# Kernel tuning notes

Measured on AMD Instinct MI355X. Metric: run time of the kernel, lower is better.

Reference implementation:

```python
import jax, jax.numpy as jnp
import numpy as np
import itertools
from jax import lax

B, DIM, RES = 32, 256, 8
KEY_DIM, NUM_HEADS, ATTN_RATIO = 16, 8, 4
NH_KD = KEY_DIM * NUM_HEADS          # 128
DH = ATTN_RATIO * KEY_DIM * NUM_HEADS  # 512
HQKV = DH + 2 * NH_KD                # 768
N = RES ** 3                         # 512


def _bias_idxs():
    pts = np.array(list(itertools.product(range(RES), repeat=3)))  # [N,3]
    off = np.abs(pts[:, None, :] - pts[None, :, :])                # [N,N,3]
    return jnp.asarray(off[..., 0] * RES * RES + off[..., 1] * RES + off[..., 2], dtype=jnp.int32)


def setup_inputs() -> dict:
    key = jax.random.key(0)
    ks = jax.random.split(key, 12)
    s = 0.05
    return {
        "x": jax.random.normal(ks[0], (B, DIM, RES, RES, RES), jnp.float32),
        "qkv_w": jax.random.normal(ks[1], (HQKV, DIM), jnp.float32) * s,
        "qkv_scale": jax.random.uniform(ks[2], (HQKV,), jnp.float32, 0.5, 1.5),
        "qkv_bias": jax.random.normal(ks[3], (HQKV,), jnp.float32) * s,
        "dw_w": jax.random.normal(ks[4], (NH_KD, 1, 3, 3, 3), jnp.float32) * s,
        "dw_scale": jax.random.uniform(ks[5], (NH_KD,), jnp.float32, 0.5, 1.5),
        "dw_bias": jax.random.normal(ks[6], (NH_KD,), jnp.float32) * s,
        "attn_biases": jax.random.normal(ks[7], (NUM_HEADS, N), jnp.float32) * s,
        "proj_w": jax.random.normal(ks[8], (DIM, DH), jnp.float32) * s,
        "proj_scale": jax.random.uniform(ks[9], (DIM,), jnp.float32, 0.5, 1.5),
        "proj_bias": jax.random.normal(ks[10], (DIM,), jnp.float32) * s,
        "bias_idxs": _bias_idxs(),
    }


def _cbn(x, w, scale, bias):
    # 1x1x1 Conv3d (pointwise, no bias) + folded BatchNorm (per-channel affine)
    y = jnp.einsum('bcdhw,oc->bodhw', x, w)
    return y * scale[None, :, None, None, None] + bias[None, :, None, None, None]


def reference(x, qkv_w, qkv_scale, qkv_bias, dw_w, dw_scale, dw_bias,
              attn_biases, proj_w, proj_scale, proj_bias, bias_idxs):
    Bx, _, D, H, W = x.shape
    n = D * H * W
    scale = KEY_DIM ** -0.5

    qkv = _cbn(x, qkv_w, qkv_scale, qkv_bias)  # [B, 768, D,H,W]
    q = qkv[:, :NH_KD]
    k = qkv[:, NH_KD:2 * NH_KD]
    v = qkv[:, 2 * NH_KD:]

    # depthwise 3x3x3 conv on q + folded BN
    q = lax.conv_general_dilated(q, dw_w, (1, 1, 1), [(1, 1)] * 3,
                                 dimension_numbers=('NCDHW', 'OIDHW', 'NCDHW'),
                                 feature_group_count=NH_KD)
    q = q * dw_scale[None, :, None, None, None] + dw_bias[None, :, None, None, None]

    q = q.reshape(Bx, NUM_HEADS, KEY_DIM, n)
    k = k.reshape(Bx, NUM_HEADS, KEY_DIM, n)
    v = v.reshape(Bx, NUM_HEADS, DH // NUM_HEADS, n)

    attn = jnp.einsum('bhcn,bhcm->bhnm', q, k) * scale
    attn = attn + attn_biases[:, bias_idxs]          # gathered rel-pos bias [h,N,N]
    attn = jax.nn.softmax(attn, axis=-1)

    out = jnp.einsum('bhdm,bhnm->bhdn', v, attn)     # v @ attn^T
    out = out.reshape(Bx, DH, D, H, W)
    out = jax.nn.relu(out)
    return _cbn(out, proj_w, proj_scale, proj_bias)
```

## Files before the change

kernel.cpp:

```cpp
#include <hip/hip_runtime.h>

typedef unsigned int u32;
typedef unsigned short u16;
typedef __attribute__((ext_vector_type(8))) short bf16x8;
typedef __attribute__((ext_vector_type(4))) float f32x4;

constexpr int BATCH = 32;
constexpr int DIM   = 256;
constexpr int NPTS  = 512;
constexpr int NH    = 8;
constexpr int KD    = 16;
constexpr int DHEAD = 64;
constexpr int NH_KD = 128;
constexpr int DH    = 512;

__device__ __forceinline__ float bflo(u32 u){ return __uint_as_float(u << 16); }
__device__ __forceinline__ float bfhi(u32 u){ return __uint_as_float(u & 0xffff0000u); }
__device__ __forceinline__ float bf2f(u16 u){ return __uint_as_float(((u32)u) << 16); }

__device__ __forceinline__ u32 pack2bf(float a, float b){
  u32 r;
  asm("v_cvt_pk_bf16_f32 %0, %1, %2" : "=v"(r) : "v"(a), "v"(b));
  return r;
}
__device__ __forceinline__ u16 f2bf(float f){ return (u16)pack2bf(f, f); }

union B8 { bf16x8 v; uint2 u2[2]; uint4 u4; };

typedef const __attribute__((address_space(1))) unsigned int gu32_t;
typedef __attribute__((address_space(3))) unsigned int su32_t;
__device__ __forceinline__ void gld16(const u16* src, u16* ldsDst){
  __builtin_amdgcn_global_load_lds((gu32_t*)src, (su32_t*)ldsDst, 16, 0, 0);
}

__global__ __launch_bounds__(256) void k_pre(
    const float* __restrict__ wq, const float* __restrict__ sq,
    const float* __restrict__ wp, const float* __restrict__ sp,
    u32* __restrict__ wqb, u32* __restrict__ pwb,
    const float* __restrict__ x, u16* __restrict__ xbt,
    const float* __restrict__ ab, const int* __restrict__ bidx,
    u32* __restrict__ biasb)
{
  __shared__ u16 T[64*68];
  const int blk = blockIdx.x;
  const int tid = threadIdx.x;

  if (blk < 640){
    int t = blk * 256 + tid;
    if (t < 98304){
      int i = 2*t;
      float s = sq[i >> 8];
      wqb[t] = pack2bf(wq[i]*s, wq[i+1]*s);
    } else {
      int j = t - 98304;
      int i = 2*j;
      float s = sp[i >> 9];
      pwb[j] = pack2bf(wp[i]*s, wp[i+1]*s);
    }
  } else if (blk < 1664){
    const int bk = blk - 640;
    const int b = bk >> 5, ct = (bk >> 3) & 3, nt = bk & 7;
    const int c0 = ct*64, n0 = nt*64;

    const float* xb = x + ((size_t)b*DIM + c0)*NPTS + n0;
    #pragma unroll
    for (int it = 0; it < 4; it++){
      int cc = (tid >> 4) + it*16;
      int nn = (tid & 15) * 4;
      float4 v = *(const float4*)(xb + (size_t)cc*NPTS + nn);
      u32* dst = (u32*)&T[cc*68 + nn];
      dst[0] = pack2bf(v.x, v.y);
      dst[1] = pack2bf(v.z, v.w);
    }
    __syncthreads();
    u16* ob = xbt + ((size_t)b*NPTS + n0)*DIM + c0;
    #pragma unroll
    for (int it = 0; it < 4; it++){
      int nn = (tid >> 4) + it*16;
      int cc = (tid & 15) * 4;
      uint2 w;
      w.x = (u32)T[(cc+0)*68 + nn] | ((u32)T[(cc+1)*68 + nn] << 16);
      w.y = (u32)T[(cc+2)*68 + nn] | ((u32)T[(cc+3)*68 + nn] << 16);
      *(uint2*)(ob + (size_t)nn*DIM + cc) = w;
    }
  } else {
    const float L2E = 1.4426950408889634f;
    const int bk = blk - 1664;
    const int mtg = bk >> 5, ntile = bk & 31;
    const int lane = tid & 63;
    const int h0 = tid >> 6;
    const int qq = lane >> 4;
    const int n = ntile*16 + (lane & 15);
    int idx[4];
    #pragma unroll
    for (int r = 0; r < 4; r++)
      idx[r] = bidx[(size_t)n*NPTS + mtg*16 + qq*4 + r];
    for (int h = h0; h < NH; h += 4){
      float v0 = ab[h*NPTS + idx[0]] * L2E, v1 = ab[h*NPTS + idx[1]] * L2E;
      float v2 = ab[h*NPTS + idx[2]] * L2E, v3 = ab[h*NPTS + idx[3]] * L2E;
      u32* dst = biasb + (((size_t)(h*32 + mtg)*32 + ntile)*64 + lane)*2;
      dst[0] = pack2bf(v0, v1);
      dst[1] = pack2bf(v2, v3);
    }
  }
}

__global__ __launch_bounds__(256) void k_qkv(
    const u16* __restrict__ xbt, const u16* __restrict__ wqb,
    const float* __restrict__ bias,
    u16* __restrict__ qfb, u16* __restrict__ kb, u16* __restrict__ vb)
{
  __shared__ u16 As[2][4096];
  __shared__ u16 Bs[2][4096];

  const int Mblk = blockIdx.x, Nblk = blockIdx.y, b = blockIdx.z;
  const int tid = threadIdx.x, wave = tid >> 6, lane = tid & 63;
  const int wm = wave >> 1, wn = wave & 1;
  const int c = lane & 15, q = lane >> 4;
  const int Mbase = Mblk*128 + wm*64;

  f32x4 acc[4][4];
  #pragma unroll
  for (int mt = 0; mt < 4; mt++){
    f32x4 bi;
    #pragma unroll
    for (int r = 0; r < 4; r++) bi[r] = bias[Mbase + mt*16 + q*4 + r];
    #pragma unroll
    for (int nt = 0; nt < 4; nt++) acc[mt][nt] = bi;
  }

  const u16* aT = wqb + (size_t)(Mblk*128)*DIM;
  const u16* bT = xbt + ((size_t)b*NPTS + Nblk*128)*DIM;

  const int srow = lane >> 2, scol = (lane & 3)*8;
  const int ch0 = wave*2;

  auto STAGE = [&](int buf, int kc){
    #pragma unroll
    for (int i = 0; i < 2; i++){
      const int ch = ch0 + i;
      gld16(aT + (size_t)(ch*16 + srow)*DIM + kc + scol, &As[buf][ch*512]);
      gld16(bT + (size_t)(ch*16 + srow)*DIM + kc + scol, &Bs[buf][ch*512]);
    }
  };

  STAGE(0, 0);
  __syncthreads();

  int cur = 0;
  #pragma unroll 2
  for (int ks = 0; ks < 8; ks++){
    if (ks < 7) STAGE(cur^1, (ks+1)*32);
    bf16x8 aW[4], bX[4];
    #pragma unroll
    for (int mt = 0; mt < 4; mt++)
      aW[mt] = *(const bf16x8*)&As[cur][(wm*64 + mt*16 + c)*32 + q*8];
    #pragma unroll
    for (int nt = 0; nt < 4; nt++)
      bX[nt] = *(const bf16x8*)&Bs[cur][(wn*64 + nt*16 + c)*32 + q*8];
    #pragma unroll
    for (int mt = 0; mt < 4; mt++)
      #pragma unroll
      for (int nt = 0; nt < 4; nt++)
        acc[mt][nt] = __builtin_amdgcn_mfma_f32_16x16x32_bf16(
            aW[mt], bX[nt], acc[mt][nt], 0, 0, 0);
    __syncthreads();
    cur ^= 1;
  }

  #pragma unroll
  for (int mt = 0; mt < 4; mt++){
    const int ob = wm*64 + mt*16 + q*4;
    #pragma unroll
    for (int nt = 0; nt < 4; nt++){
      const int n = Nblk*128 + wn*64 + nt*16 + c;
      #pragma unroll
      for (int r = 0; r < 4; r++){
        u16 bv = f2bf(acc[mt][nt][r]);
        int ol = ob + r;
        if (Mblk == 0){
          qfb[((size_t)b*NH_KD + ol)*NPTS + n] = bv;
        } else if (Mblk == 1){
          kb[(((size_t)b*NH + (ol >> 4))*NPTS + n)*16 + (ol & 15)] = bv;
        } else {
          int d = (Mblk - 2)*128 + ol;
          int p = (n & ~31) | (n & 3) | (((n >> 4) & 1) << 2) | (((n >> 2) & 3) << 3);
          vb[((size_t)b*DH + d)*NPTS + p] = bv;
        }
      }
    }
  }
}

__global__ __launch_bounds__(512) void k_dw(
    const u16* __restrict__ qfb, const float* __restrict__ dww,
    const float* __restrict__ dws, const float* __restrict__ dwb,
    u16* __restrict__ qb)
{
  const int bc = blockIdx.x;
  const int b  = bc >> 7;
  const int ch = bc & 127;
  const int n  = threadIdx.x;
  const int z = n >> 6, y = (n >> 3) & 7, xx = n & 7;
  float wv[27];
  #pragma unroll
  for (int i = 0; i < 27; i++) wv[i] = dww[ch*27 + i];
  const u16* qp = qfb + (size_t)bc * NPTS;
  float acc = 0.f;
  #pragma unroll
  for (int dz = 0; dz < 3; dz++){
    int zz = z + dz - 1; if ((unsigned)zz > 7u) continue;
    #pragma unroll
    for (int dy = 0; dy < 3; dy++){
      int yy = y + dy - 1; if ((unsigned)yy > 7u) continue;
      #pragma unroll
      for (int dx = 0; dx < 3; dx++){
        int xw = xx + dx - 1; if ((unsigned)xw > 7u) continue;
        acc += bf2f(qp[zz*64 + yy*8 + xw]) * wv[dz*9 + dy*3 + dx];
      }
    }
  }
  acc = (acc * dws[ch] + dwb[ch]) * 0.36067376022224085f;
  int hh = ch >> 4, cc = ch & 15;
  qb[(((size_t)b*NH + hh)*NPTS + n)*16 + cc] = f2bf(acc);
}

__global__ __launch_bounds__(256, 4) void k_attn(
    const u16* __restrict__ qb, const u16* __restrict__ kb,
    const u16* __restrict__ vb, const u16* __restrict__ biasb,
    u16* __restrict__ attnout)
{
  __shared__ u16 VS[2][64][40];

  const int hb = blockIdx.x, tg = blockIdx.y;
  const int b = hb >> 3, h = hb & 7;
  const int tid = threadIdx.x;
  const int lane = tid & 63, wave = tid >> 6;
  const int c = lane & 15, q = lane >> 4;
  const int bh = b*NH + h;
  const int nt0 = tg*8 + wave*2;
  const int n0 = nt0*16;

  const int vr = tid >> 2;
  const int vc = (tid & 3) * 8;

  const bf16x8 zfrag = {0,0,0,0,0,0,0,0};
  bf16x8 bQ0 = zfrag, bQ1 = zfrag;
  if (q < 2){
    bQ0 = *(const bf16x8*)(qb + (((size_t)bh*NPTS + n0 + c) << 4) + q*8);
    bQ1 = *(const bf16x8*)(qb + (((size_t)bh*NPTS + n0 + 16 + c) << 4) + q*8);
  }

  const u16* kbh = kb + ((size_t)bh*NPTS)*16;
  const u16* vbh = vb + ((size_t)b*DH + h*DHEAD)*NPTS;
  const u16* bw0 = biasb + (size_t)h*262144 + (size_t)nt0*256 + lane*4;

  f32x4 O0[4] = {{0,0,0,0},{0,0,0,0},{0,0,0,0},{0,0,0,0}};
  f32x4 O1[4] = {{0,0,0,0},{0,0,0,0},{0,0,0,0},{0,0,0,0}};
  float ls0 = 0.f, ls1 = 0.f;

  bf16x8 aK0, aK1;
  uint2 u00, u01, u10, u11;

  auto loadKB = [&](int win, bf16x8& k0, bf16x8& k1,
                    uint2& x00, uint2& x01, uint2& x10, uint2& x11){
    const int mtg = win*2;
    if (q < 2){
      k0 = *(const bf16x8*)(kbh + (((size_t)(mtg*16 + c)) << 4) + q*8);
      k1 = *(const bf16x8*)(kbh + (((size_t)(mtg*16 + 16 + c)) << 4) + q*8);
    } else { k0 = zfrag; k1 = zfrag; }
    x00 = *(const uint2*)(bw0 + (size_t)mtg*8192);
    x01 = *(const uint2*)(bw0 + (size_t)(mtg+1)*8192);
    x10 = *(const uint2*)(bw0 + 256 + (size_t)mtg*8192);
    x11 = *(const uint2*)(bw0 + 256 + (size_t)(mtg+1)*8192);
  };

  {
    bf16x8 sv = *(const bf16x8*)(vbh + (size_t)vr*NPTS + vc);
    *(bf16x8*)&VS[0][vr][vc] = sv;
  }
  loadKB(0, aK0, aK1, u00, u01, u10, u11);
  __syncthreads();

  #pragma unroll 1
  for (int win = 0; win < 16; win++){
    const int wnext = (win < 15) ? win + 1 : 15;
    bf16x8 sv = *(const bf16x8*)(vbh + (size_t)vr*NPTS + wnext*32 + vc);

    bf16x8 nK0, nK1;
    uint2 m00, m01, m10, m11;
    if (win < 15)
      loadKB(win+1, nK0, nK1, m00, m01, m10, m11);

    const int vbuf = win & 1;
    bf16x8 V0 = *(const bf16x8*)&VS[vbuf][ 0 + c][q*8];
    bf16x8 V1 = *(const bf16x8*)&VS[vbuf][16 + c][q*8];
    bf16x8 V2 = *(const bf16x8*)&VS[vbuf][32 + c][q*8];
    bf16x8 V3 = *(const bf16x8*)&VS[vbuf][48 + c][q*8];

    f32x4 c00, c01, c10, c11;
    c00[0]=bflo(u00.x); c00[1]=bfhi(u00.x); c00[2]=bflo(u00.y); c00[3]=bfhi(u00.y);
    c01[0]=bflo(u01.x); c01[1]=bfhi(u01.x); c01[2]=bflo(u01.y); c01[3]=bfhi(u01.y);
    c10[0]=bflo(u10.x); c10[1]=bfhi(u10.x); c10[2]=bflo(u10.y); c10[3]=bfhi(u10.y);
    c11[0]=bflo(u11.x); c11[1]=bfhi(u11.x); c11[2]=bflo(u11.y); c11[3]=bfhi(u11.y);
    f32x4 S00 = __builtin_amdgcn_mfma_f32_16x16x32_bf16(aK0, bQ0, c00, 0, 0, 0);
    f32x4 S01 = __builtin_amdgcn_mfma_f32_16x16x32_bf16(aK1, bQ0, c01, 0, 0, 0);
    f32x4 S10 = __builtin_amdgcn_mfma_f32_16x16x32_bf16(aK0, bQ1, c10, 0, 0, 0);
    f32x4 S11 = __builtin_amdgcn_mfma_f32_16x16x32_bf16(aK1, bQ1, c11, 0, 0, 0);

    float e0, e1, e2, e3;
    B8 aP0, aP1;
    e0 = __builtin_amdgcn_exp2f(S00[0]); e1 = __builtin_amdgcn_exp2f(S00[1]);
    e2 = __builtin_amdgcn_exp2f(S00[2]); e3 = __builtin_amdgcn_exp2f(S00[3]);
    ls0 += (e0 + e1) + (e2 + e3);
    aP0.u4.x = pack2bf(e0, e1); aP0.u4.y = pack2bf(e2, e3);
    e0 = __builtin_amdgcn_exp2f(S01[0]); e1 = __builtin_amdgcn_exp2f(S01[1]);
    e2 = __builtin_amdgcn_exp2f(S01[2]); e3 = __builtin_amdgcn_exp2f(S01[3]);
    ls0 += (e0 + e1) + (e2 + e3);
    aP0.u4.z = pack2bf(e0, e1); aP0.u4.w = pack2bf(e2, e3);
    e0 = __builtin_amdgcn_exp2f(S10[0]); e1 = __builtin_amdgcn_exp2f(S10[1]);
    e2 = __builtin_amdgcn_exp2f(S10[2]); e3 = __builtin_amdgcn_exp2f(S10[3]);
    ls1 += (e0 + e1) + (e2 + e3);
    aP1.u4.x = pack2bf(e0, e1); aP1.u4.y = pack2bf(e2, e3);
    e0 = __builtin_amdgcn_exp2f(S11[0]); e1 = __builtin_amdgcn_exp2f(S11[1]);
    e2 = __builtin_amdgcn_exp2f(S11[2]); e3 = __builtin_amdgcn_exp2f(S11[3]);
    ls1 += (e0 + e1) + (e2 + e3);
    aP1.u4.z = pack2bf(e0, e1); aP1.u4.w = pack2bf(e2, e3);

    O0[0] = __builtin_amdgcn_mfma_f32_16x16x32_bf16(aP0.v, V0, O0[0], 0, 0, 0);
    O1[0] = __builtin_amdgcn_mfma_f32_16x16x32_bf16(aP1.v, V0, O1[0], 0, 0, 0);
    O0[1] = __builtin_amdgcn_mfma_f32_16x16x32_bf16(aP0.v, V1, O0[1], 0, 0, 0);
    O1[1] = __builtin_amdgcn_mfma_f32_16x16x32_bf16(aP1.v, V1, O1[1], 0, 0, 0);
    O0[2] = __builtin_amdgcn_mfma_f32_16x16x32_bf16(aP0.v, V2, O0[2], 0, 0, 0);
    O1[2] = __builtin_amdgcn_mfma_f32_16x16x32_bf16(aP1.v, V2, O1[2], 0, 0, 0);
    O0[3] = __builtin_amdgcn_mfma_f32_16x16x32_bf16(aP0.v, V3, O0[3], 0, 0, 0);
    O1[3] = __builtin_amdgcn_mfma_f32_16x16x32_bf16(aP1.v, V3, O1[3], 0, 0, 0);

    if (win < 15)
      *(bf16x8*)&VS[wnext & 1][vr][vc] = sv;
    __syncthreads();

    aK0 = nK0; aK1 = nK1;
    u00 = m00; u01 = m01; u10 = m10; u11 = m11;
  }

  ls0 += __shfl_xor(ls0, 16, 64);
  ls0 += __shfl_xor(ls0, 32, 64);
  ls1 += __shfl_xor(ls1, 16, 64);
  ls1 += __shfl_xor(ls1, 32, 64);
  f32x4 inv0, inv1;
  #pragma unroll
  for (int r = 0; r < 4; r++){
    inv0[r] = 1.0f / __shfl(ls0, q*4 + r, 64);
    inv1[r] = 1.0f / __shfl(ls1, q*4 + r, 64);
  }

  u16* ao = attnout + ((size_t)(b*NPTS + n0))*DH + h*DHEAD;
  #pragma unroll
  for (int dt = 0; dt < 4; dt++)
    #pragma unroll
    for (int r = 0; r < 4; r++){
      ao[(size_t)(q*4 + r)*DH + dt*16 + c] =
          f2bf(fmaxf(O0[dt][r]*inv0[r], 0.f));
      ao[(size_t)(16 + q*4 + r)*DH + dt*16 + c] =
          f2bf(fmaxf(O1[dt][r]*inv1[r], 0.f));
    }
}

__global__ __launch_bounds__(256) void k_proj(
    const u16* __restrict__ attn, const u16* __restrict__ pwb,
    const float* __restrict__ bias, float* __restrict__ out)
{
  __shared__ u16 As[2][4096];
  __shared__ u16 Bs[2][4096];

  const int Mblk = blockIdx.x, Nblk = blockIdx.y, b = blockIdx.z;
  const int tid = threadIdx.x, wave = tid >> 6, lane = tid & 63;
  const int wm = wave >> 1, wn = wave & 1;
  const int c = lane & 15, q = lane >> 4;
  const int Mbase = Mblk*128 + wm*64;

  f32x4 acc[4][4];
  #pragma unroll
  for (int mt = 0; mt < 4; mt++){
    f32x4 bi;
    #pragma unroll
    for (int r = 0; r < 4; r++) bi[r] = bias[Mbase + mt*16 + q*4 + r];
    #pragma unroll
    for (int nt = 0; nt < 4; nt++) acc[mt][nt] = bi;
  }

  const u16* aT = pwb + (size_t)(Mblk*128)*DH;
  const u16* bT = attn + ((size_t)b*NPTS + Nblk*128)*DH;

  const int srow = lane >> 2, scol = (lane & 3)*8;
  const int ch0 = wave*2;

  auto STAGE = [&](int buf, int kc){
    #pragma unroll
    for (int i = 0; i < 2; i++){
      const int ch = ch0 + i;
      gld16(aT + (size_t)(ch*16 + srow)*DH + kc + scol, &As[buf][ch*512]);
      gld16(bT + (size_t)(ch*16 + srow)*DH + kc + scol, &Bs[buf][ch*512]);
    }
  };

  STAGE(0, 0);
  __syncthreads();

  int cur = 0;
  #pragma unroll 2
  for (int ks = 0; ks < 16; ks++){
    if (ks < 15) STAGE(cur^1, (ks+1)*32);
    bf16x8 aW[4], bA[4];
    #pragma unroll
    for (int mt = 0; mt < 4; mt++)
      aW[mt] = *(const bf16x8*)&As[cur][(wm*64 + mt*16 + c)*32 + q*8];
    #pragma unroll
    for (int nt = 0; nt < 4; nt++)
      bA[nt] = *(const bf16x8*)&Bs[cur][(wn*64 + nt*16 + c)*32 + q*8];
    #pragma unroll
    for (int mt = 0; mt < 4; mt++)
      #pragma unroll
      for (int nt = 0; nt < 4; nt++)
        acc[mt][nt] = __builtin_amdgcn_mfma_f32_16x16x32_bf16(
            aW[mt], bA[nt], acc[mt][nt], 0, 0, 0);
    __syncthreads();
    cur ^= 1;
  }

  #pragma unroll
  for (int mt = 0; mt < 4; mt++){
    #pragma unroll
    for (int nt = 0; nt < 4; nt++){
      const int n = Nblk*128 + wn*64 + nt*16 + c;
      #pragma unroll
      for (int r = 0; r < 4; r++){
        int o = Mbase + mt*16 + q*4 + r;
        out[((size_t)b*DIM + o)*NPTS + n] = acc[mt][nt][r];
      }
    }
  }
}

extern "C" void kernel_launch(void* const* d_in, const int* in_sizes, int n_in,
                              void* d_out, int out_size, void* d_ws, size_t ws_size,
                              hipStream_t stream)
{
  const float* x     = (const float*)d_in[0];
  const float* qkv_w = (const float*)d_in[1];
  const float* qkv_s = (const float*)d_in[2];
  const float* qkv_b = (const float*)d_in[3];
  const float* dw_w  = (const float*)d_in[4];
  const float* dw_s  = (const float*)d_in[5];
  const float* dw_b  = (const float*)d_in[6];
  const float* ab    = (const float*)d_in[7];
  const float* pw    = (const float*)d_in[8];
  const float* ps    = (const float*)d_in[9];
  const float* pb    = (const float*)d_in[10];
  const int* bidx    = (const int*)d_in[11];

  char* ws = (char*)d_ws;
  u16*   qfb   = (u16*)  (ws);
  u16*   qb    = (u16*)  (ws + ( 4u << 20));
  u16*   kb    = (u16*)  (ws + ( 8u << 20));
  u16*   vb    = (u16*)  (ws + (12u << 20));
  u16*   attn  = (u16*)  (ws + (28u << 20));
  u32*   biasb = (u32*)  (ws + (44u << 20));
  u32*   wqb   = (u32*)  (ws + (48u << 20));
  u32*   pwb   = (u32*)  (ws + (49u << 20));
  u16*   xbt   = (u16*)  (ws + (50u << 20));

  k_pre <<<dim3(2688),     256, 0, stream>>>(qkv_w, qkv_s, pw, ps, wqb, pwb,
                                             x, xbt, ab, bidx, biasb);
  k_qkv <<<dim3(6, 4, 32), 256, 0, stream>>>(xbt, (const u16*)wqb, qkv_b, qfb, kb, vb);
  k_dw  <<<dim3(32*128),   512, 0, stream>>>(qfb, dw_w, dw_s, dw_b, qb);
  k_attn<<<dim3(256, 4),   256, 0, stream>>>(qb, kb, vb, (const u16*)biasb, attn);
  k_proj<<<dim3(2, 4, 32), 256, 0, stream>>>(attn, (const u16*)pwb, pb, (float*)d_out);
}
```

Before: 186.8 us.

## Vectorize GEMM epilogue stores via quad transpose, remap blocks per XCD, drop LDS in qkv

The qkv and proj GEMM epilogues now transpose 4x4 accumulator fragments across lane quads with shuffles, so each lane writes a contiguous 8- or 16-byte vector instead of scattered scalar stores. Both GEMMs switch to a 1-D grid whose block index is remapped so blocks sharing the same batch and N-tile land on the same XCD, which should improve L2 reuse of the x and attn tiles. k_qkv also drops its LDS double buffering and loads MFMA operands straight from global memory, relying on the cache. This removes LDS traffic and barriers but exposes global-load latency inside the K loop.

```diff
diff --git a/kernel.cpp b/kernel.cpp
--- a/kernel.cpp
+++ b/kernel.cpp
@@ -31,6 +31,18 @@
 typedef __attribute__((address_space(3))) unsigned int su32_t;
 __device__ __forceinline__ void gld16(const u16* src, u16* ldsDst){
   __builtin_amdgcn_global_load_lds((gu32_t*)src, (su32_t*)ldsDst, 16, 0, 0);
+}
+
+__device__ __forceinline__ void quadtr(float v[4], int lq){
+  float t[4], y[4];
+  #pragma unroll
+  for (int r = 0; r < 4; r++) t[r] = __shfl_xor(v[r], 1, 64);
+  #pragma unroll
+  for (int r = 0; r < 4; r++) y[r] = ((r & 1) == (lq & 1)) ? v[r] : t[r ^ 1];
+  #pragma unroll
+  for (int r = 0; r < 4; r++) t[r] = __shfl_xor(y[r], 2, 64);
+  #pragma unroll
+  for (int r = 0; r < 4; r++) v[r] = ((r & 2) == (lq & 2)) ? y[r] : t[r ^ 2];
 }
 
 __global__ __launch_bounds__(256) void k_pre(
@@ -110,14 +122,20 @@
     const float* __restrict__ bias,
     u16* __restrict__ qfb, u16* __restrict__ kb, u16* __restrict__ vb)
 {
-  __shared__ u16 As[2][4096];
-  __shared__ u16 Bs[2][4096];
-
-  const int Mblk = blockIdx.x, Nblk = blockIdx.y, b = blockIdx.z;
+  const int blk = blockIdx.x;
+  const int xcd = blk & 7;
+  const int idx = blk >> 3;
+  const int pair = xcd*16 + idx/6;
+  const int Mblk = idx % 6;
+  const int Nblk = pair & 3;
+  const int b    = pair >> 2;
+
   const int tid = threadIdx.x, wave = tid >> 6, lane = tid & 63;
   const int wm = wave >> 1, wn = wave & 1;
   const int c = lane & 15, q = lane >> 4;
+  const int lq = lane & 3;
   const int Mbase = Mblk*128 + wm*64;
+  const int Nbase = Nblk*128 + wn*64;
 
   f32x4 acc[4][4];
   #pragma unroll
@@ -129,63 +147,52 @@
     for (int nt = 0; nt < 4; nt++) acc[mt][nt] = bi;
   }
 
-  const u16* aT = wqb + (size_t)(Mblk*128)*DIM;
-  const u16* bT = xbt + ((size_t)b*NPTS + Nblk*128)*DIM;
-
-  const int srow = lane >> 2, scol = (lane & 3)*8;
-  const int ch0 = wave*2;
-
-  auto STAGE = [&](int buf, int kc){
-    #pragma unroll
-    for (int i = 0; i < 2; i++){
-      const int ch = ch0 + i;
-      gld16(aT + (size_t)(ch*16 + srow)*DIM + kc + scol, &As[buf][ch*512]);
-      gld16(bT + (size_t)(ch*16 + srow)*DIM + kc + scol, &Bs[buf][ch*512]);
-    }
-  };
-
-  STAGE(0, 0);
-  __syncthreads();
-
-  int cur = 0;
-  #pragma unroll 2
-  for (int ks = 0; ks < 8; ks++){
-    if (ks < 7) STAGE(cur^1, (ks+1)*32);
+  const u16* xrow = xbt + (size_t)b*NPTS*DIM;
+
+  for (int kc8 = 0; kc8 < 8; kc8++){
+    const int kc = kc8*32;
     bf16x8 aW[4], bX[4];
     #pragma unroll
     for (int mt = 0; mt < 4; mt++)
-      aW[mt] = *(const bf16x8*)&As[cur][(wm*64 + mt*16 + c)*32 + q*8];
+      aW[mt] = *(const bf16x8*)(wqb + (size_t)(Mbase + mt*16 + c)*DIM + kc + q*8);
     #pragma unroll
     for (int nt = 0; nt < 4; nt++)
-      bX[nt] = *(const bf16x8*)&Bs[cur][(wn*64 + nt*16 + c)*32 + q*8];
+      bX[nt] = *(const bf16x8*)(xrow + (size_t)(Nbase + nt*16 + c)*DIM + kc + q*8);
     #pragma unroll
     for (int mt = 0; mt < 4; mt++)
       #pragma unroll
       for (int nt = 0; nt < 4; nt++)
         acc[mt][nt] = __builtin_amdgcn_mfma_f32_16x16x32_bf16(
             aW[mt], bX[nt], acc[mt][nt], 0, 0, 0);
-    __syncthreads();
-    cur ^= 1;
   }
 
   #pragma unroll
   for (int mt = 0; mt < 4; mt++){
-    const int ob = wm*64 + mt*16 + q*4;
+    const int m0 = wm*64 + mt*16 + q*4;
     #pragma unroll
     for (int nt = 0; nt < 4; nt++){
-      const int n = Nblk*128 + wn*64 + nt*16 + c;
-      #pragma unroll
-      for (int r = 0; r < 4; r++){
-        u16 bv = f2bf(acc[mt][nt][r]);
-        int ol = ob + r;
+      if (Mblk == 1){
+        const int n = Nbase + nt*16 + c;
+        const int hh = wm*4 + mt;
+        uint2 w;
+        w.x = pack2bf(acc[mt][nt][0], acc[mt][nt][1]);
+        w.y = pack2bf(acc[mt][nt][2], acc[mt][nt][3]);
+        *(uint2*)(kb + (((size_t)b*NH + hh)*NPTS + n)*16 + q*4) = w;
+      } else {
+        float v[4];
+        #pragma unroll
+        for (int r = 0; r < 4; r++) v[r] = acc[mt][nt][r];
+        quadtr(v, lq);
+        const int nq = Nbase + nt*16 + (c & ~3);
+        uint2 w;
+        w.x = pack2bf(v[0], v[1]);
+        w.y = pack2bf(v[2], v[3]);
         if (Mblk == 0){
-          qfb[((size_t)b*NH_KD + ol)*NPTS + n] = bv;
-        } else if (Mblk == 1){
-          kb[(((size_t)b*NH + (ol >> 4))*NPTS + n)*16 + (ol & 15)] = bv;
+          *(uint2*)(qfb + ((size_t)b*NH_KD + m0 + lq)*NPTS + nq) = w;
         } else {
-          int d = (Mblk - 2)*128 + ol;
-          int p = (n & ~31) | (n & 3) | (((n >> 4) & 1) << 2) | (((n >> 2) & 3) << 3);
-          vb[((size_t)b*DH + d)*NPTS + p] = bv;
+          const int d = (Mblk - 2)*128 + m0 + lq;
+          const int pb = (nq & ~31) | (((nq >> 4) & 1) << 2) | (((nq >> 2) & 3) << 3);
+          *(uint2*)(vb + ((size_t)b*DH + d)*NPTS + pb) = w;
         }
       }
     }
@@ -374,10 +381,18 @@
   __shared__ u16 As[2][4096];
   __shared__ u16 Bs[2][4096];
 
-  const int Mblk = blockIdx.x, Nblk = blockIdx.y, b = blockIdx.z;
+  const int blk = blockIdx.x;
+  const int xcd = blk & 7;
+  const int idx = blk >> 3;
+  const int pair = xcd*16 + (idx >> 1);
+  const int Mblk = idx & 1;
+  const int Nblk = pair & 3;
+  const int b    = pair >> 2;
+
   const int tid = threadIdx.x, wave = tid >> 6, lane = tid & 63;
   const int wm = wave >> 1, wn = wave & 1;
   const int c = lane & 15, q = lane >> 4;
+  const int lq = lane & 3;
   const int Mbase = Mblk*128 + wm*64;
 
   f32x4 acc[4][4];
@@ -431,14 +446,16 @@
 
   #pragma unroll
   for (int mt = 0; mt < 4; mt++){
+    const int o0 = Mbase + mt*16 + q*4;
     #pragma unroll
     for (int nt = 0; nt < 4; nt++){
-      const int n = Nblk*128 + wn*64 + nt*16 + c;
+      float v[4];
       #pragma unroll
-      for (int r = 0; r < 4; r++){
-        int o = Mbase + mt*16 + q*4 + r;
-        out[((size_t)b*DIM + o)*NPTS + n] = acc[mt][nt][r];
-      }
+      for (int r = 0; r < 4; r++) v[r] = acc[mt][nt][r];
+      quadtr(v, lq);
+      const int nq = Nblk*128 + wn*64 + nt*16 + (c & ~3);
+      float4 w; w.x = v[0]; w.y = v[1]; w.z = v[2]; w.w = v[3];
+      *(float4*)(out + ((size_t)b*DIM + o0 + lq)*NPTS + nq) = w;
     }
   }
 }
@@ -473,8 +490,8 @@
 
   k_pre <<<dim3(2688),     256, 0, stream>>>(qkv_w, qkv_s, pw, ps, wqb, pwb,
                                              x, xbt, ab, bidx, biasb);
-  k_qkv <<<dim3(6, 4, 32), 256, 0, stream>>>(xbt, (const u16*)wqb, qkv_b, qfb, kb, vb);
+  k_qkv <<<dim3(768),      256, 0, stream>>>(xbt, (const u16*)wqb, qkv_b, qfb, kb, vb);
   k_dw  <<<dim3(32*128),   512, 0, stream>>>(qfb, dw_w, dw_s, dw_b, qb);
   k_attn<<<dim3(256, 4),   256, 0, stream>>>(qb, kb, vb, (const u16*)biasb, attn);
-  k_proj<<<dim3(2, 4, 32), 256, 0, stream>>>(attn, (const u16*)pwb, pb, (float*)d_out);
-}
+  k_proj<<<dim3(256),      256, 0, stream>>>(attn, (const u16*)pwb, pb, (float*)d_out);
+}
```

Measured after the change: 185.9 us. Within noise of the previous version (-0.5%).
